# Kernel optimization log

Measured on AMD Instinct MI355X. Metric: run time of the kernel, lower is better.

The kernel has to match this reference:

```python
import jax, jax.numpy as jnp
import numpy as np

CH, HEADS, DH, NMEM, GROUPS, EPS = 128, 4, 32, 4, 32, 1e-5
HID = HEADS * DH

def group_norm(x, w, b):
    # x: [B,C,D,H,W], normalize per group of channels over (C//G, D, H, W)
    B, C = x.shape[0], x.shape[1]
    xg = x.reshape(B, GROUPS, -1)
    mu = xg.mean(axis=-1, keepdims=True)
    var = xg.var(axis=-1, keepdims=True)
    xg = (xg - mu) * jax.lax.rsqrt(var + EPS)
    x = xg.reshape(x.shape)
    return x * w[None, :, None, None, None] + b[None, :, None, None, None]

def setup_inputs() -> dict:
    key = jax.random.key(0)
    ks = jax.random.split(key, 8)
    B, D, H, W = 2, 16, 64, 64
    x = jax.random.normal(ks[0], (B, CH, D, H, W), dtype=jnp.float32)
    norm1_w = jnp.ones((CH,), jnp.float32)
    norm1_b = jnp.zeros((CH,), jnp.float32)
    w_qkv = jax.random.normal(ks[1], (3 * HID, CH), dtype=jnp.float32) * (CH ** -0.5)
    mem_kv = jax.random.normal(ks[2], (2, HEADS, DH, NMEM), dtype=jnp.float32)
    w_out = jax.random.normal(ks[3], (CH, HID), dtype=jnp.float32) * (HID ** -0.5)
    b_out = jnp.zeros((CH,), jnp.float32)
    norm2_w = jnp.ones((CH,), jnp.float32)
    norm2_b = jnp.zeros((CH,), jnp.float32)
    return {"x": x, "norm1_w": norm1_w, "norm1_b": norm1_b, "w_qkv": w_qkv,
            "mem_kv": mem_kv, "w_out": w_out, "b_out": b_out,
            "norm2_w": norm2_w, "norm2_b": norm2_b}

def reference(x, norm1_w, norm1_b, w_qkv, mem_kv, w_out, b_out, norm2_w, norm2_b):
    B, C, D, H, W = x.shape
    n = D * H * W
    scale = DH ** -0.5
    xn = group_norm(x, norm1_w, norm1_b)
    # 1x1x1 conv == channel matmul: [B,3*HID,n]
    qkv = jnp.einsum('oc,bcn->bon', w_qkv, xn.reshape(B, C, n))
    qkv = qkv.reshape(B, 3, HEADS, DH, n)
    q, k, v = qkv[:, 0], qkv[:, 1], qkv[:, 2]  # [B,HEADS,DH,n]
    mk = jnp.broadcast_to(mem_kv[0][None], (B, HEADS, DH, NMEM))
    mv = jnp.broadcast_to(mem_kv[1][None], (B, HEADS, DH, NMEM))
    k = jnp.concatenate([mk, k], axis=-1)
    v = jnp.concatenate([mv, v], axis=-1)
    q = jax.nn.softmax(q, axis=-2) * scale   # over dim_head
    k = jax.nn.softmax(k, axis=-1)           # over sequence
    context = jnp.einsum('bhdn,bhen->bhde', k, v)  # [B,HEADS,DH,DH]
    out = jnp.einsum('bhde,bhdn->bhen', context, q)  # [B,HEADS,DH,n]
    out = out.reshape(B, HID, D, H, W)
    out = jnp.einsum('oc,bcdhw->bodhw', w_out, out) + b_out[None, :, None, None, None]
    return group_norm(out, norm2_w, norm2_b)
```

## Files before the change

kernel.cpp:

```cpp
#include <hip/hip_runtime.h>
#include <math.h>

#define CH     128
#define EPSV   1e-5f
#define SCALE  0.17677669529663687f
#define GSIZE  262144.0f

typedef short bf16x8 __attribute__((ext_vector_type(8)));
typedef short bf16x4 __attribute__((ext_vector_type(4)));
typedef float f32x4  __attribute__((ext_vector_type(4)));

__device__ __forceinline__ unsigned cvtpk(float lo, float hi) {
    unsigned r;
    asm("v_cvt_pk_bf16_f32 %0, %1, %2" : "=v"(r) : "v"(lo), "v"(hi));
    return r;
}
__device__ __forceinline__ unsigned short f2bf(float f) {
    unsigned u = __float_as_uint(f);
    u += 0x7FFF + ((u >> 16) & 1);
    return (unsigned short)(u >> 16);
}
__device__ __forceinline__ float bf2f(unsigned short s) {
    return __uint_as_float(((unsigned)s) << 16);
}

__global__ __launch_bounds__(256) void gn_partial(const float* __restrict__ x,
                                                  float* __restrict__ part) {
    __shared__ float s1[256], s2[256];
    int t = threadIdx.x;
    const float4* xp = (const float4*)(x + (size_t)blockIdx.x * 8192);
    float s = 0.f, q = 0.f;
#pragma unroll
    for (int i = 0; i < 8; ++i) {
        float4 v = xp[t + 256 * i];
        s += v.x + v.y + v.z + v.w;
        q += v.x * v.x + v.y * v.y + v.z * v.z + v.w * v.w;
    }
    s1[t] = s; s2[t] = q;
    __syncthreads();
    for (int st = 128; st > 0; st >>= 1) {
        if (t < st) { s1[t] += s1[t + st]; s2[t] += s2[t + st]; }
        __syncthreads();
    }
    if (t == 0) { part[2 * blockIdx.x] = s1[0]; part[2 * blockIdx.x + 1] = s2[0]; }
}

__global__ void prep1(const float* __restrict__ part, float* __restrict__ mu, float* __restrict__ rs) {
    int t = threadIdx.x;
    float s = 0.f, q = 0.f;
    for (int i = 0; i < 32; ++i) { s += part[2*(t*32+i)]; q += part[2*(t*32+i)+1]; }
    float m = s * (1.f / GSIZE);
    float v = q * (1.f / GSIZE) - m * m;
    mu[t] = m; rs[t] = rsqrtf(v + EPSV);
}

__global__ __launch_bounds__(256) void kv_pass(const float* __restrict__ x,
        const float* __restrict__ w_qkv,
        const float* __restrict__ n1w, const float* __restrict__ n1b,
        const float* __restrict__ mu, const float* __restrict__ rs,
        float* __restrict__ part_kv) {
    __shared__ short xk[16*64*8];
    __shared__ short kvstage[8*256*8];
    int tid = threadIdx.x;
    int l = tid & 63, w = tid >> 6;
    int ncol = l & 15, kg = l >> 4;
    int b = blockIdx.x >> 8;
    int h = w;

    bf16x8 afrag[4][4];
    {
        int row0 = 128 + w*64 + ncol;
        int k0   = 8 * kg;
#pragma unroll
        for (int rt = 0; rt < 4; ++rt)
#pragma unroll
        for (int ks = 0; ks < 4; ++ks) {
            const float* p = w_qkv + (size_t)(row0 + 16*rt)*CH + k0 + 32*ks;
            float4 u0 = *(const float4*)p;
            float4 u1 = *(const float4*)(p + 4);
            bf16x8 f;
            f[0]=(short)f2bf(u0.x); f[1]=(short)f2bf(u0.y); f[2]=(short)f2bf(u0.z); f[3]=(short)f2bf(u0.w);
            f[4]=(short)f2bf(u1.x); f[5]=(short)f2bf(u1.y); f[6]=(short)f2bf(u1.z); f[7]=(short)f2bf(u1.w);
            afrag[rt][ks] = f;
        }
    }

    int nst = (tid & 15) * 4;
    int cst = (tid >> 4) * 8;
    float aa[8], bb[8];
#pragma unroll
    for (int i = 0; i < 8; ++i) {
        int c = cst + i;
        int fg = b*32 + (c >> 2);
        float a0 = rs[fg] * n1w[c];
        aa[i] = a0;
        bb[i] = n1b[c] - mu[fg] * a0;
    }

    f32x4 cc[2][2];
#pragma unroll
    for (int i = 0; i < 2; ++i)
#pragma unroll
    for (int j = 0; j < 2; ++j)
#pragma unroll
    for (int q = 0; q < 4; ++q) cc[i][j][q] = 0.f;
    float zacc[2] = {0.f, 0.f};

    float4 xv[8];
    {
        int n0 = ((blockIdx.x * 4) << 6) & 65535;
#pragma unroll
        for (int i = 0; i < 8; ++i)
            xv[i] = *(const float4*)(x + ((size_t)(b*CH + cst + i) << 16) + n0 + nst);
        const float* xf = (const float*)xv;
#pragma unroll
        for (int j = 0; j < 4; ++j) {
            bf16x8 f;
#pragma unroll
            for (int i = 0; i < 8; ++i)
                f[i] = (short)f2bf(xf[i*4 + j] * aa[i] + bb[i]);
            *(bf16x8*)&xk[((cst >> 3)*64 + nst + j) * 8] = f;
        }
    }

    for (int t4 = 0; t4 < 4; ++t4) {
        __syncthreads();

        f32x4 acc[4][4];
#pragma unroll
        for (int i = 0; i < 4; ++i)
#pragma unroll
        for (int j = 0; j < 4; ++j)
#pragma unroll
        for (int q = 0; q < 4; ++q) acc[i][j][q] = 0.f;

#pragma unroll
        for (int ks = 0; ks < 4; ++ks) {
            bf16x8 bfr[4];
#pragma unroll
            for (int ct = 0; ct < 4; ++ct)
                bfr[ct] = *(bf16x8*)&xk[((4*ks + kg)*64 + 16*ct + ncol) * 8];
#pragma unroll
            for (int rt = 0; rt < 4; ++rt)
#pragma unroll
            for (int ct = 0; ct < 4; ++ct)
                acc[rt][ct] = __builtin_amdgcn_mfma_f32_16x16x32_bf16(
                    afrag[rt][ks], bfr[ct], acc[rt][ct], 0, 0, 0);
        }

#pragma unroll
        for (int rt = 0; rt < 4; ++rt)
#pragma unroll
        for (int ct = 0; ct < 4; ++ct) {
            float v0 = acc[rt][ct][0], v1 = acc[rt][ct][1];
            float v2 = acc[rt][ct][2], v3 = acc[rt][ct][3];
            if (w < 2) { v0 = __expf(v0); v1 = __expf(v1); v2 = __expf(v2); v3 = __expf(v3); }
            unsigned p01 = cvtpk(v0, v1), p23 = cvtpk(v2, v3);
            unsigned short sv[4] = {(unsigned short)p01, (unsigned short)(p01 >> 16),
                                    (unsigned short)p23, (unsigned short)(p23 >> 16)};
            int n = 16*ct + ncol;
#pragma unroll
            for (int q = 0; q < 4; ++q) {
                int row = w*64 + 16*rt + 4*kg + q;
                int byteoff = ((n >> 3)*4096 + row*16 + (n & 7)*2) ^ (((row >> 2) & 3) << 4);
                *(unsigned short*)((char*)kvstage + byteoff) = sv[q];
            }
        }
        __syncthreads();

        if (t4 < 3) {
            int n0 = ((blockIdx.x * 4 + t4 + 1) << 6) & 65535;
#pragma unroll
            for (int i = 0; i < 8; ++i)
                xv[i] = *(const float4*)(x + ((size_t)(b*CH + cst + i) << 16) + n0 + nst);
        }

#pragma unroll
        for (int ks = 0; ks < 2; ++ks) {
            bf16x8 ak[2], bv[2];
#pragma unroll
            for (int rt = 0; rt < 2; ++rt) {
                int row = h*32 + 16*rt + ncol;
                int byteoff = ((4*ks + kg)*4096 + row*16) ^ (((row >> 2) & 3) << 4);
                ak[rt] = *(bf16x8*)((char*)kvstage + byteoff);
            }
#pragma unroll
            for (int ct = 0; ct < 2; ++ct) {
                int row = 128 + h*32 + 16*ct + ncol;
                int byteoff = ((4*ks + kg)*4096 + row*16) ^ (((row >> 2) & 3) << 4);
                bv[ct] = *(bf16x8*)((char*)kvstage + byteoff);
            }
#pragma unroll
            for (int rt = 0; rt < 2; ++rt)
#pragma unroll
            for (int j = 0; j < 8; ++j) zacc[rt] += bf2f((unsigned short)ak[rt][j]);
#pragma unroll
            for (int rt = 0; rt < 2; ++rt)
#pragma unroll
            for (int ct = 0; ct < 2; ++ct)
                cc[rt][ct] = __builtin_amdgcn_mfma_f32_16x16x32_bf16(
                    ak[rt], bv[ct], cc[rt][ct], 0, 0, 0);
        }

        if (t4 < 3) {
            const float* xf = (const float*)xv;
#pragma unroll
            for (int j = 0; j < 4; ++j) {
                bf16x8 f;
#pragma unroll
                for (int i = 0; i < 8; ++i)
                    f[i] = (short)f2bf(xf[i*4 + j] * aa[i] + bb[i]);
                *(bf16x8*)&xk[((cst >> 3)*64 + nst + j) * 8] = f;
            }
        }
    }

    float* dst = part_kv + (size_t)blockIdx.x * 4224;
#pragma unroll
    for (int rt = 0; rt < 2; ++rt)
#pragma unroll
    for (int ct = 0; ct < 2; ++ct)
#pragma unroll
    for (int q = 0; q < 4; ++q) {
        int d = 16*rt + 4*kg + q;
        int e = 16*ct + ncol;
        dst[h*1024 + d*32 + e] = cc[rt][ct][q];
    }
#pragma unroll
    for (int rt = 0; rt < 2; ++rt) {
        zacc[rt] += __shfl_xor(zacc[rt], 16);
        zacc[rt] += __shfl_xor(zacc[rt], 32);
    }
    if (kg == 0) {
        dst[4096 + h*32 + ncol]      = zacc[0];
        dst[4096 + h*32 + 16 + ncol] = zacc[1];
    }
}

__global__ __launch_bounds__(256) void reduce_ctx(const float* __restrict__ part_kv,
                                                  const float* __restrict__ mem_kv,
                                                  float* __restrict__ ctx, float* __restrict__ Z) {
    int gid = blockIdx.x * 256 + threadIdx.x;
    int oi = gid >> 2, sub = gid & 3;
    int b = oi / 4224;
    int e = oi - b * 4224;
    const float* p = part_kv + (size_t)b * 256 * 4224 + e;
    float s = 0.f;
    for (int i = sub; i < 256; i += 4) s += p[(size_t)i * 4224];
    s += __shfl_xor(s, 1);
    s += __shfl_xor(s, 2);
    if (sub == 0) {
        if (e < 4096) {
            int hh = e >> 10, d = (e >> 5) & 31, ee = e & 31;
            float init = 0.f;
            for (int m = 0; m < 4; ++m)
                init += expf(mem_kv[hh*128 + d*4 + m]) * mem_kv[512 + hh*128 + ee*4 + m];
            ctx[b*4096 + e] = init + s;
        } else {
            int d2 = e - 4096;
            float init = 0.f;
            for (int m = 0; m < 4; ++m) init += expf(mem_kv[d2*4 + m]);
            Z[b*128 + d2] = init + s;
        }
    }
}

template<bool BF16OUT>
__global__ __launch_bounds__(256) void out_pass(const float* __restrict__ x,
        const float* __restrict__ w_qkv,
        const float* __restrict__ n1w, const float* __restrict__ n1b,
        const float* __restrict__ mu, const float* __restrict__ rs,
        const float* __restrict__ ctx, const float* __restrict__ Z,
        const float* __restrict__ w_out, const float* __restrict__ b_out,
        float* __restrict__ out, unsigned short* __restrict__ outb,
        float* __restrict__ part2) {
    __shared__ short xk[16*64*8];
    __shared__ short pb[16*64*8];
    int tid = threadIdx.x;
    int l = tid & 63, w = tid >> 6;
    int ncol = l & 15, kg = l >> 4;
    int b = blockIdx.x >> 8;

    bf16x8 aq[2][4], aw[2][4];
#pragma unroll
    for (int rt = 0; rt < 2; ++rt)
#pragma unroll
    for (int ks = 0; ks < 4; ++ks) {
        const float* pq = w_qkv + (size_t)(32*w + 16*rt + ncol)*CH + 8*kg + 32*ks;
        const float* pw = w_out + (size_t)(32*w + 16*rt + ncol)*CH + 8*kg + 32*ks;
        float4 u0 = *(const float4*)pq, u1 = *(const float4*)(pq + 4);
        float4 v0 = *(const float4*)pw, v1 = *(const float4*)(pw + 4);
        bf16x8 fq, fw;
        fq[0]=(short)f2bf(u0.x); fq[1]=(short)f2bf(u0.y); fq[2]=(short)f2bf(u0.z); fq[3]=(short)f2bf(u0.w);
        fq[4]=(short)f2bf(u1.x); fq[5]=(short)f2bf(u1.y); fq[6]=(short)f2bf(u1.z); fq[7]=(short)f2bf(u1.w);
        fw[0]=(short)f2bf(v0.x); fw[1]=(short)f2bf(v0.y); fw[2]=(short)f2bf(v0.z); fw[3]=(short)f2bf(v0.w);
        fw[4]=(short)f2bf(v1.x); fw[5]=(short)f2bf(v1.y); fw[6]=(short)f2bf(v1.z); fw[7]=(short)f2bf(v1.w);
        aq[rt][ks] = fq;
        aw[rt][ks] = fw;
    }

    bf16x8 actx[2];
#pragma unroll
    for (int rt = 0; rt < 2; ++rt) {
        bf16x8 f;
#pragma unroll
        for (int j = 0; j < 8; ++j) {
            int d = 8*kg + j;
            float cv = ctx[b*4096 + w*1024 + d*32 + 16*rt + ncol] / Z[b*128 + w*32 + d];
            f[j] = (short)f2bf(cv);
        }
        actx[rt] = f;
    }

    float bo[2][4];
#pragma unroll
    for (int rt = 0; rt < 2; ++rt)
#pragma unroll
    for (int q = 0; q < 4; ++q)
        bo[rt][q] = b_out[32*w + 16*rt + 4*kg + q];

    int nst = (tid & 15) * 4;
    int cst = (tid >> 4) * 8;
    float aa[8], bb[8];
#pragma unroll
    for (int i = 0; i < 8; ++i) {
        int c = cst + i;
        int fg = b*32 + (c >> 2);
        float a0 = rs[fg] * n1w[c];
        aa[i] = a0;
        bb[i] = n1b[c] - mu[fg] * a0;
    }

    float pgs[2] = {0.f, 0.f}, pgq[2] = {0.f, 0.f};
    float4 xv[8];

    {
        int n0 = (blockIdx.x << 8) & 65535;
#pragma unroll
        for (int i = 0; i < 8; ++i)
            xv[i] = *(const float4*)(x + ((size_t)(b*CH + cst + i) << 16) + n0 + nst);
        const float* xf = (const float*)xv;
#pragma unroll
        for (int j = 0; j < 4; ++j) {
            bf16x8 f;
#pragma unroll
            for (int i = 0; i < 8; ++i)
                f[i] = (short)f2bf(xf[i*4 + j] * aa[i] + bb[i]);
            *(bf16x8*)&xk[((cst >> 3)*64 + nst + j) * 8] = f;
        }
    }

    for (int t4 = 0; t4 < 4; ++t4) {
        int n0 = ((blockIdx.x*4 + t4) << 6) & 65535;
        __syncthreads();

        f32x4 acc[2][4];
#pragma unroll
        for (int i = 0; i < 2; ++i)
#pragma unroll
        for (int j = 0; j < 4; ++j)
#pragma unroll
        for (int q = 0; q < 4; ++q) acc[i][j][q] = 0.f;
#pragma unroll
        for (int ks = 0; ks < 4; ++ks) {
            bf16x8 bfr[4];
#pragma unroll
            for (int ct = 0; ct < 4; ++ct)
                bfr[ct] = *(bf16x8*)&xk[((4*ks + kg)*64 + 16*ct + ncol) * 8];
#pragma unroll
            for (int rt = 0; rt < 2; ++rt)
#pragma unroll
            for (int ct = 0; ct < 4; ++ct)
                acc[rt][ct] = __builtin_amdgcn_mfma_f32_16x16x32_bf16(
                    aq[rt][ks], bfr[ct], acc[rt][ct], 0, 0, 0);
        }

        {
            float sum[4];
#pragma unroll
            for (int ct = 0; ct < 4; ++ct) {
                float s = 0.f;
#pragma unroll
                for (int rt = 0; rt < 2; ++rt)
#pragma unroll
                for (int q = 0; q < 4; ++q) {
                    float e = __expf(acc[rt][ct][q]);
                    acc[rt][ct][q] = e;
                    s += e;
                }
                s += __shfl_xor(s, 16);
                s += __shfl_xor(s, 32);
                sum[ct] = SCALE / s;
            }
#pragma unroll
            for (int ct = 0; ct < 4; ++ct)
#pragma unroll
            for (int rt = 0; rt < 2; ++rt) {
                bf16x4 pk;
#pragma unroll
                for (int q = 0; q < 4; ++q) pk[q] = (short)f2bf(acc[rt][ct][q] * sum[ct]);
                int row0 = w*32 + 16*rt + 4*kg;
                *(bf16x4*)&pb[((row0 >> 3)*64 + 16*ct + ncol)*8 + (row0 & 7)] = pk;
            }
        }

        f32x4 hacc[2][4];
#pragma unroll
        for (int i = 0; i < 2; ++i)
#pragma unroll
        for (int j = 0; j < 4; ++j)
#pragma unroll
        for (int q = 0; q < 4; ++q) hacc[i][j][q] = 0.f;
        {
            bf16x8 bq[4];
#pragma unroll
            for (int ct = 0; ct < 4; ++ct)
                bq[ct] = *(bf16x8*)&pb[((w*4 + kg)*64 + 16*ct + ncol) * 8];
#pragma unroll
            for (int rt = 0; rt < 2; ++rt)
#pragma unroll
            for (int ct = 0; ct < 4; ++ct)
                hacc[rt][ct] = __builtin_amdgcn_mfma_f32_16x16x32_bf16(
                    actx[rt], bq[ct], hacc[rt][ct], 0, 0, 0);
        }

#pragma unroll
        for (int ct = 0; ct < 4; ++ct)
#pragma unroll
        for (int rt = 0; rt < 2; ++rt) {
            bf16x4 pk;
#pragma unroll
            for (int q = 0; q < 4; ++q) pk[q] = (short)f2bf(hacc[rt][ct][q]);
            int row0 = w*32 + 16*rt + 4*kg;
            *(bf16x4*)&pb[((row0 >> 3)*64 + 16*ct + ncol)*8 + (row0 & 7)] = pk;
        }
        __syncthreads();

        if (t4 < 3) {
            int n1 = ((blockIdx.x*4 + t4 + 1) << 6) & 65535;
#pragma unroll
            for (int i = 0; i < 8; ++i)
                xv[i] = *(const float4*)(x + ((size_t)(b*CH + cst + i) << 16) + n1 + nst);
        }

        f32x4 oacc[2][4];
#pragma unroll
        for (int i = 0; i < 2; ++i)
#pragma unroll
        for (int j = 0; j < 4; ++j)
#pragma unroll
        for (int q = 0; q < 4; ++q) oacc[i][j][q] = 0.f;
#pragma unroll
        for (int ks = 0; ks < 4; ++ks) {
            bf16x8 bfr[4];
#pragma unroll
            for (int ct = 0; ct < 4; ++ct)
                bfr[ct] = *(bf16x8*)&pb[((4*ks + kg)*64 + 16*ct + ncol) * 8];
#pragma unroll
            for (int rt = 0; rt < 2; ++rt)
#pragma unroll
            for (int ct = 0; ct < 4; ++ct)
                oacc[rt][ct] = __builtin_amdgcn_mfma_f32_16x16x32_bf16(
                    aw[rt][ks], bfr[ct], oacc[rt][ct], 0, 0, 0);
        }

#pragma unroll
        for (int rt = 0; rt < 2; ++rt)
#pragma unroll
        for (int ct = 0; ct < 4; ++ct)
#pragma unroll
        for (int q = 0; q < 4; ++q) {
            int c = 32*w + 16*rt + 4*kg + q;
            float o = oacc[rt][ct][q] + bo[rt][q];
            size_t idx = ((size_t)(b*CH + c) << 16) + n0 + 16*ct + ncol;
            if (BF16OUT) outb[idx] = f2bf(o);
            else         out[idx] = o;
            pgs[rt] += o;
            pgq[rt] += o*o;
        }

        if (t4 < 3) {
            const float* xf = (const float*)xv;
#pragma unroll
            for (int j = 0; j < 4; ++j) {
                bf16x8 f;
#pragma unroll
                for (int i = 0; i < 8; ++i)
                    f[i] = (short)f2bf(xf[i*4 + j] * aa[i] + bb[i]);
                *(bf16x8*)&xk[((cst >> 3)*64 + nst + j) * 8] = f;
            }
        }
    }

#pragma unroll
    for (int rt = 0; rt < 2; ++rt) {
        float gs = pgs[rt], gq = pgq[rt];
#pragma unroll
        for (int m = 1; m < 16; m <<= 1) {
            gs += __shfl_xor(gs, m);
            gq += __shfl_xor(gq, m);
        }
        if (ncol == 0) {
            int g = 8*w + 4*rt + kg;
            part2[blockIdx.x*64 + g*2 + 0] = gs;
            part2[blockIdx.x*64 + g*2 + 1] = gq;
        }
    }
}

__global__ __launch_bounds__(256) void reduce2(const float* __restrict__ part2,
                                               float* __restrict__ mu, float* __restrict__ rs) {
    __shared__ float s1[256], s2[256];
    int fg = blockIdx.x;
    int b = fg >> 5, g = fg & 31;
    int t = threadIdx.x;
    const float* p = part2 + ((size_t)(b*256 + t))*64 + g*2;
    s1[t] = p[0]; s2[t] = p[1];
    __syncthreads();
    for (int st = 128; st > 0; st >>= 1) {
        if (t < st) { s1[t] += s1[t + st]; s2[t] += s2[t + st]; }
        __syncthreads();
    }
    if (t == 0) {
        float m = s1[0] * (1.f / GSIZE);
        float v = s2[0] * (1.f / GSIZE) - m*m;
        mu[fg] = m; rs[fg] = rsqrtf(v + EPSV);
    }
}

__global__ __launch_bounds__(256) void gn_apply(float* __restrict__ y,
        const float* __restrict__ mu, const float* __restrict__ rs,
        const float* __restrict__ w2, const float* __restrict__ b2) {
    int bi = blockIdx.x, t = threadIdx.x;
    int c = (bi >> 3) & 127;
    int b = bi >> 10;
    int fg = b*32 + (c >> 2);
    float aa = rs[fg] * w2[c];
    float bb = b2[c] - mu[fg] * aa;
    float4* yp = (float4*)(y + (size_t)bi * 8192);
#pragma unroll
    for (int i = 0; i < 8; ++i) {
        float4 v = yp[t + 256*i];
        v.x = v.x*aa+bb; v.y = v.y*aa+bb; v.z = v.z*aa+bb; v.w = v.w*aa+bb;
        yp[t + 256*i] = v;
    }
}

__global__ __launch_bounds__(256) void gn_apply_bf16(const unsigned short* __restrict__ src,
        float* __restrict__ y,
        const float* __restrict__ mu, const float* __restrict__ rs,
        const float* __restrict__ w2, const float* __restrict__ b2) {
    int bi = blockIdx.x, t = threadIdx.x;
    int c = (bi >> 3) & 127;
    int b = bi >> 10;
    int fg = b*32 + (c >> 2);
    float aa = rs[fg] * w2[c];
    float bb = b2[c] - mu[fg] * aa;
    const ushort4* sp = (const ushort4*)(src + (size_t)bi * 8192);
    float4* yp = (float4*)(y + (size_t)bi * 8192);
#pragma unroll
    for (int i = 0; i < 8; ++i) {
        ushort4 u = sp[t + 256*i];
        float4 v;
        v.x = bf2f(u.x)*aa+bb; v.y = bf2f(u.y)*aa+bb;
        v.z = bf2f(u.z)*aa+bb; v.w = bf2f(u.w)*aa+bb;
        yp[t + 256*i] = v;
    }
}

extern "C" void kernel_launch(void* const* d_in, const int* in_sizes, int n_in,
                              void* d_out, int out_size, void* d_ws, size_t ws_size,
                              hipStream_t stream) {
    (void)in_sizes; (void)n_in; (void)out_size;
    const float* x      = (const float*)d_in[0];
    const float* n1w    = (const float*)d_in[1];
    const float* n1b    = (const float*)d_in[2];
    const float* w_qkv  = (const float*)d_in[3];
    const float* mem_kv = (const float*)d_in[4];
    const float* w_out  = (const float*)d_in[5];
    const float* b_out  = (const float*)d_in[6];
    const float* n2w    = (const float*)d_in[7];
    const float* n2b    = (const float*)d_in[8];
    float* out = (float*)d_out;
    float* ws  = (float*)d_ws;

    float* part1   = ws;
    float* mu1     = ws + 4096;
    float* rs1     = ws + 4160;
    float* ctx     = ws + 4224;
    float* Z       = ws + 12416;
    float* part2   = ws + 12672;
    float* mu2     = ws + 143744;
    float* rs2     = ws + 143808;
    float* part_kv = ws + 143872;
    const size_t base_floats = 143872 + (size_t)512*4224;
    unsigned short* outb = (unsigned short*)(ws + base_floats);
    const size_t need = base_floats*4 + (size_t)2*CH*65536*2;
    bool bf16path = ws_size >= need;

    gn_partial<<<2048, 256, 0, stream>>>(x, part1);
    prep1<<<1, 64, 0, stream>>>(part1, mu1, rs1);
    kv_pass<<<512, 256, 0, stream>>>(x, w_qkv, n1w, n1b, mu1, rs1, part_kv);
    reduce_ctx<<<132, 256, 0, stream>>>(part_kv, mem_kv, ctx, Z);
    if (bf16path) {
        out_pass<true><<<512, 256, 0, stream>>>(x, w_qkv, n1w, n1b, mu1, rs1, ctx, Z,
                                                w_out, b_out, out, outb, part2);
        reduce2<<<64, 256, 0, stream>>>(part2, mu2, rs2);
        gn_apply_bf16<<<2048, 256, 0, stream>>>(outb, out, mu2, rs2, n2w, n2b);
    } else {
        out_pass<false><<<512, 256, 0, stream>>>(x, w_qkv, n1w, n1b, mu1, rs1, ctx, Z,
                                                 w_out, b_out, out, outb, part2);
        reduce2<<<64, 256, 0, stream>>>(part2, mu2, rs2);
        gn_apply<<<2048, 256, 0, stream>>>(out, mu2, rs2, n2w, n2b);
    }
}
```

Measured before the change: 135.3 us.

## Fold GroupNorm affine into QKV weights and per-row bias; use packed bf16 converts

The per-channel GroupNorm scale is folded into the bf16 QKV weight fragments, and the shift becomes a per-output-row bias computed once per block and kept in shared memory. The raw x tile then only needs a packed bf16 conversion per element instead of an FMA plus manual rounding, and the bias is added to the MFMA accumulators before exp/softmax. Manual f2bf rounding is replaced by the hardware v_cvt_pk_bf16_f32 packed convert in several places. The trade-off is extra setup work per block, a small shared array, and slightly different rounding, since unnormalized x and scaled weights are quantized to bf16 separately, which could lose accuracy when group statistics are large.

```diff
diff --git a/kernel.cpp b/kernel.cpp
--- a/kernel.cpp
+++ b/kernel.cpp
@@ -14,6 +14,16 @@
     unsigned r;
     asm("v_cvt_pk_bf16_f32 %0, %1, %2" : "=v"(r) : "v"(lo), "v"(hi));
     return r;
+}
+__device__ __forceinline__ bf16x4 pk4(unsigned p01, unsigned p23) {
+    union { unsigned u[2]; bf16x4 v; } t;
+    t.u[0] = p01; t.u[1] = p23;
+    return t.v;
+}
+__device__ __forceinline__ bf16x8 pk8(unsigned a, unsigned b, unsigned c, unsigned d) {
+    union { unsigned u[4]; bf16x8 v; } t;
+    t.u[0] = a; t.u[1] = b; t.u[2] = c; t.u[3] = d;
+    return t.v;
 }
 __device__ __forceinline__ unsigned short f2bf(float f) {
     unsigned u = __float_as_uint(f);
@@ -61,6 +71,7 @@
         float* __restrict__ part_kv) {
     __shared__ short xk[16*64*8];
     __shared__ short kvstage[8*256*8];
+    __shared__ float betas[256];
     int tid = threadIdx.x;
     int l = tid & 63, w = tid >> 6;
     int ncol = l & 15, kg = l >> 4;
@@ -68,34 +79,41 @@
     int h = w;
 
     bf16x8 afrag[4][4];
-    {
-        int row0 = 128 + w*64 + ncol;
-        int k0   = 8 * kg;
-#pragma unroll
-        for (int rt = 0; rt < 4; ++rt)
-#pragma unroll
-        for (int ks = 0; ks < 4; ++ks) {
-            const float* p = w_qkv + (size_t)(row0 + 16*rt)*CH + k0 + 32*ks;
-            float4 u0 = *(const float4*)p;
-            float4 u1 = *(const float4*)(p + 4);
-            bf16x8 f;
-            f[0]=(short)f2bf(u0.x); f[1]=(short)f2bf(u0.y); f[2]=(short)f2bf(u0.z); f[3]=(short)f2bf(u0.w);
-            f[4]=(short)f2bf(u1.x); f[5]=(short)f2bf(u1.y); f[6]=(short)f2bf(u1.z); f[7]=(short)f2bf(u1.w);
-            afrag[rt][ks] = f;
-        }
+    float bsum[4] = {0.f, 0.f, 0.f, 0.f};
+#pragma unroll
+    for (int ks = 0; ks < 4; ++ks) {
+        float a0[8], b0[8];
+#pragma unroll
+        for (int j = 0; j < 8; ++j) {
+            int c = 8*kg + 32*ks + j;
+            int fg = b*32 + (c >> 2);
+            float av = rs[fg] * n1w[c];
+            a0[j] = av;
+            b0[j] = n1b[c] - mu[fg] * av;
+        }
+#pragma unroll
+        for (int rt = 0; rt < 4; ++rt) {
+            const float* p = w_qkv + (size_t)(128 + w*64 + 16*rt + ncol)*CH + 8*kg + 32*ks;
+            float4 u0 = *(const float4*)p, u1 = *(const float4*)(p + 4);
+            float wv[8] = {u0.x,u0.y,u0.z,u0.w,u1.x,u1.y,u1.z,u1.w};
+            afrag[rt][ks] = pk8(cvtpk(wv[0]*a0[0], wv[1]*a0[1]), cvtpk(wv[2]*a0[2], wv[3]*a0[3]),
+                                cvtpk(wv[4]*a0[4], wv[5]*a0[5]), cvtpk(wv[6]*a0[6], wv[7]*a0[7]));
+#pragma unroll
+            for (int j = 0; j < 8; ++j) bsum[rt] += wv[j] * b0[j];
+        }
+    }
+#pragma unroll
+    for (int rt = 0; rt < 4; ++rt) {
+        bsum[rt] += __shfl_xor(bsum[rt], 16);
+        bsum[rt] += __shfl_xor(bsum[rt], 32);
+    }
+    if (kg == 0) {
+#pragma unroll
+        for (int rt = 0; rt < 4; ++rt) betas[w*64 + 16*rt + ncol] = bsum[rt];
     }
 
     int nst = (tid & 15) * 4;
     int cst = (tid >> 4) * 8;
-    float aa[8], bb[8];
-#pragma unroll
-    for (int i = 0; i < 8; ++i) {
-        int c = cst + i;
-        int fg = b*32 + (c >> 2);
-        float a0 = rs[fg] * n1w[c];
-        aa[i] = a0;
-        bb[i] = n1b[c] - mu[fg] * a0;
-    }
 
     f32x4 cc[2][2];
 #pragma unroll
@@ -114,13 +132,10 @@
             xv[i] = *(const float4*)(x + ((size_t)(b*CH + cst + i) << 16) + n0 + nst);
         const float* xf = (const float*)xv;
 #pragma unroll
-        for (int j = 0; j < 4; ++j) {
-            bf16x8 f;
-#pragma unroll
-            for (int i = 0; i < 8; ++i)
-                f[i] = (short)f2bf(xf[i*4 + j] * aa[i] + bb[i]);
-            *(bf16x8*)&xk[((cst >> 3)*64 + nst + j) * 8] = f;
-        }
+        for (int j = 0; j < 4; ++j)
+            *(bf16x8*)&xk[((cst >> 3)*64 + nst + j) * 8] =
+                pk8(cvtpk(xf[0*4+j], xf[1*4+j]), cvtpk(xf[2*4+j], xf[3*4+j]),
+                    cvtpk(xf[4*4+j], xf[5*4+j]), cvtpk(xf[6*4+j], xf[7*4+j]));
     }
 
     for (int t4 = 0; t4 < 4; ++t4) {
@@ -149,21 +164,25 @@
         }
 
 #pragma unroll
-        for (int rt = 0; rt < 4; ++rt)
-#pragma unroll
-        for (int ct = 0; ct < 4; ++ct) {
-            float v0 = acc[rt][ct][0], v1 = acc[rt][ct][1];
-            float v2 = acc[rt][ct][2], v3 = acc[rt][ct][3];
-            if (w < 2) { v0 = __expf(v0); v1 = __expf(v1); v2 = __expf(v2); v3 = __expf(v3); }
-            unsigned p01 = cvtpk(v0, v1), p23 = cvtpk(v2, v3);
-            unsigned short sv[4] = {(unsigned short)p01, (unsigned short)(p01 >> 16),
-                                    (unsigned short)p23, (unsigned short)(p23 >> 16)};
-            int n = 16*ct + ncol;
-#pragma unroll
-            for (int q = 0; q < 4; ++q) {
-                int row = w*64 + 16*rt + 4*kg + q;
-                int byteoff = ((n >> 3)*4096 + row*16 + (n & 7)*2) ^ (((row >> 2) & 3) << 4);
-                *(unsigned short*)((char*)kvstage + byteoff) = sv[q];
+        for (int rt = 0; rt < 4; ++rt) {
+            int lrow0 = w*64 + 16*rt + 4*kg;
+            float be0 = betas[lrow0+0], be1 = betas[lrow0+1];
+            float be2 = betas[lrow0+2], be3 = betas[lrow0+3];
+#pragma unroll
+            for (int ct = 0; ct < 4; ++ct) {
+                float v0 = acc[rt][ct][0] + be0, v1 = acc[rt][ct][1] + be1;
+                float v2 = acc[rt][ct][2] + be2, v3 = acc[rt][ct][3] + be3;
+                if (w < 2) { v0 = __expf(v0); v1 = __expf(v1); v2 = __expf(v2); v3 = __expf(v3); }
+                unsigned p01 = cvtpk(v0, v1), p23 = cvtpk(v2, v3);
+                unsigned short sv[4] = {(unsigned short)p01, (unsigned short)(p01 >> 16),
+                                        (unsigned short)p23, (unsigned short)(p23 >> 16)};
+                int n = 16*ct + ncol;
+#pragma unroll
+                for (int q = 0; q < 4; ++q) {
+                    int row = lrow0 + q;
+                    int byteoff = ((n >> 3)*4096 + row*16 + (n & 7)*2) ^ (((row >> 2) & 3) << 4);
+                    *(unsigned short*)((char*)kvstage + byteoff) = sv[q];
+                }
             }
         }
         __syncthreads();
@@ -205,13 +224,10 @@
         if (t4 < 3) {
             const float* xf = (const float*)xv;
 #pragma unroll
-            for (int j = 0; j < 4; ++j) {
-                bf16x8 f;
-#pragma unroll
-                for (int i = 0; i < 8; ++i)
-                    f[i] = (short)f2bf(xf[i*4 + j] * aa[i] + bb[i]);
-                *(bf16x8*)&xk[((cst >> 3)*64 + nst + j) * 8] = f;
-            }
+            for (int j = 0; j < 4; ++j)
+                *(bf16x8*)&xk[((cst >> 3)*64 + nst + j) * 8] =
+                    pk8(cvtpk(xf[0*4+j], xf[1*4+j]), cvtpk(xf[2*4+j], xf[3*4+j]),
+                        cvtpk(xf[4*4+j], xf[5*4+j]), cvtpk(xf[6*4+j], xf[7*4+j]));
         }
     }
 
@@ -276,27 +292,49 @@
         float* __restrict__ part2) {
     __shared__ short xk[16*64*8];
     __shared__ short pb[16*64*8];
+    __shared__ float betasq[128];
     int tid = threadIdx.x;
     int l = tid & 63, w = tid >> 6;
     int ncol = l & 15, kg = l >> 4;
     int b = blockIdx.x >> 8;
 
     bf16x8 aq[2][4], aw[2][4];
-#pragma unroll
-    for (int rt = 0; rt < 2; ++rt)
+    float bsq[2] = {0.f, 0.f};
 #pragma unroll
     for (int ks = 0; ks < 4; ++ks) {
-        const float* pq = w_qkv + (size_t)(32*w + 16*rt + ncol)*CH + 8*kg + 32*ks;
-        const float* pw = w_out + (size_t)(32*w + 16*rt + ncol)*CH + 8*kg + 32*ks;
-        float4 u0 = *(const float4*)pq, u1 = *(const float4*)(pq + 4);
-        float4 v0 = *(const float4*)pw, v1 = *(const float4*)(pw + 4);
-        bf16x8 fq, fw;
-        fq[0]=(short)f2bf(u0.x); fq[1]=(short)f2bf(u0.y); fq[2]=(short)f2bf(u0.z); fq[3]=(short)f2bf(u0.w);
-        fq[4]=(short)f2bf(u1.x); fq[5]=(short)f2bf(u1.y); fq[6]=(short)f2bf(u1.z); fq[7]=(short)f2bf(u1.w);
-        fw[0]=(short)f2bf(v0.x); fw[1]=(short)f2bf(v0.y); fw[2]=(short)f2bf(v0.z); fw[3]=(short)f2bf(v0.w);
-        fw[4]=(short)f2bf(v1.x); fw[5]=(short)f2bf(v1.y); fw[6]=(short)f2bf(v1.z); fw[7]=(short)f2bf(v1.w);
-        aq[rt][ks] = fq;
-        aw[rt][ks] = fw;
+        float a0[8], b0[8];
+#pragma unroll
+        for (int j = 0; j < 8; ++j) {
+            int c = 8*kg + 32*ks + j;
+            int fg = b*32 + (c >> 2);
+            float av = rs[fg] * n1w[c];
+            a0[j] = av;
+            b0[j] = n1b[c] - mu[fg] * av;
+        }
+#pragma unroll
+        for (int rt = 0; rt < 2; ++rt) {
+            const float* pq = w_qkv + (size_t)(32*w + 16*rt + ncol)*CH + 8*kg + 32*ks;
+            const float* pw = w_out + (size_t)(32*w + 16*rt + ncol)*CH + 8*kg + 32*ks;
+            float4 u0 = *(const float4*)pq, u1 = *(const float4*)(pq + 4);
+            float4 v0 = *(const float4*)pw, v1 = *(const float4*)(pw + 4);
+            float wq[8] = {u0.x,u0.y,u0.z,u0.w,u1.x,u1.y,u1.z,u1.w};
+            float wo[8] = {v0.x,v0.y,v0.z,v0.w,v1.x,v1.y,v1.z,v1.w};
+            aq[rt][ks] = pk8(cvtpk(wq[0]*a0[0], wq[1]*a0[1]), cvtpk(wq[2]*a0[2], wq[3]*a0[3]),
+                             cvtpk(wq[4]*a0[4], wq[5]*a0[5]), cvtpk(wq[6]*a0[6], wq[7]*a0[7]));
+            aw[rt][ks] = pk8(cvtpk(wo[0], wo[1]), cvtpk(wo[2], wo[3]),
+                             cvtpk(wo[4], wo[5]), cvtpk(wo[6], wo[7]));
+#pragma unroll
+            for (int j = 0; j < 8; ++j) bsq[rt] += wq[j] * b0[j];
+        }
+    }
+#pragma unroll
+    for (int rt = 0; rt < 2; ++rt) {
+        bsq[rt] += __shfl_xor(bsq[rt], 16);
+        bsq[rt] += __shfl_xor(bsq[rt], 32);
+    }
+    if (kg == 0) {
+#pragma unroll
+        for (int rt = 0; rt < 2; ++rt) betasq[32*w + 16*rt + ncol] = bsq[rt];
     }
 
     bf16x8 actx[2];
@@ -321,16 +359,6 @@
 
     int nst = (tid & 15) * 4;
     int cst = (tid >> 4) * 8;
-    float aa[8], bb[8];
-#pragma unroll
-    for (int i = 0; i < 8; ++i) {
-        int c = cst + i;
-        int fg = b*32 + (c >> 2);
-        float a0 = rs[fg] * n1w[c];
-        aa[i] = a0;
-        bb[i] = n1b[c] - mu[fg] * a0;
-    }
-
     float pgs[2] = {0.f, 0.f}, pgq[2] = {0.f, 0.f};
     float4 xv[8];
 
@@ -341,13 +369,10 @@
             xv[i] = *(const float4*)(x + ((size_t)(b*CH + cst + i) << 16) + n0 + nst);
         const float* xf = (const float*)xv;
 #pragma unroll
-        for (int j = 0; j < 4; ++j) {
-            bf16x8 f;
-#pragma unroll
-            for (int i = 0; i < 8; ++i)
-                f[i] = (short)f2bf(xf[i*4 + j] * aa[i] + bb[i]);
-            *(bf16x8*)&xk[((cst >> 3)*64 + nst + j) * 8] = f;
-        }
+        for (int j = 0; j < 4; ++j)
+            *(bf16x8*)&xk[((cst >> 3)*64 + nst + j) * 8] =
+                pk8(cvtpk(xf[0*4+j], xf[1*4+j]), cvtpk(xf[2*4+j], xf[3*4+j]),
+                    cvtpk(xf[4*4+j], xf[5*4+j]), cvtpk(xf[6*4+j], xf[7*4+j]));
     }
 
     for (int t4 = 0; t4 < 4; ++t4) {
@@ -376,6 +401,11 @@
         }
 
         {
+            float be[2][4];
+#pragma unroll
+            for (int rt = 0; rt < 2; ++rt)
+#pragma unroll
+            for (int q = 0; q < 4; ++q) be[rt][q] = betasq[32*w + 16*rt + 4*kg + q];
             float sum[4];
 #pragma unroll
             for (int ct = 0; ct < 4; ++ct) {
@@ -384,7 +414,7 @@
                 for (int rt = 0; rt < 2; ++rt)
 #pragma unroll
                 for (int q = 0; q < 4; ++q) {
-                    float e = __expf(acc[rt][ct][q]);
+                    float e = __expf(acc[rt][ct][q] + be[rt][q]);
                     acc[rt][ct][q] = e;
                     s += e;
                 }
@@ -396,11 +426,10 @@
             for (int ct = 0; ct < 4; ++ct)
 #pragma unroll
             for (int rt = 0; rt < 2; ++rt) {
-                bf16x4 pk;
-#pragma unroll
-                for (int q = 0; q < 4; ++q) pk[q] = (short)f2bf(acc[rt][ct][q] * sum[ct]);
+                unsigned p01 = cvtpk(acc[rt][ct][0]*sum[ct], acc[rt][ct][1]*sum[ct]);
+                unsigned p23 = cvtpk(acc[rt][ct][2]*sum[ct], acc[rt][ct][3]*sum[ct]);
                 int row0 = w*32 + 16*rt + 4*kg;
-                *(bf16x4*)&pb[((row0 >> 3)*64 + 16*ct + ncol)*8 + (row0 & 7)] = pk;
+                *(bf16x4*)&pb[((row0 >> 3)*64 + 16*ct + ncol)*8 + (row0 & 7)] = pk4(p01, p23);
             }
         }
 
@@ -428,11 +457,10 @@
         for (int ct = 0; ct < 4; ++ct)
 #pragma unroll
         for (int rt = 0; rt < 2; ++rt) {
-            bf16x4 pk;
-#pragma unroll
-            for (int q = 0; q < 4; ++q) pk[q] = (short)f2bf(hacc[rt][ct][q]);
+            unsigned p01 = cvtpk(hacc[rt][ct][0], hacc[rt][ct][1]);
+            unsigned p23 = cvtpk(hacc[rt][ct][2], hacc[rt][ct][3]);
             int row0 = w*32 + 16*rt + 4*kg;
-            *(bf16x4*)&pb[((row0 >> 3)*64 + 16*ct + ncol)*8 + (row0 & 7)] = pk;
+            *(bf16x4*)&pb[((row0 >> 3)*64 + 16*ct + ncol)*8 + (row0 & 7)] = pk4(p01, p23);
         }
         __syncthreads();
 
@@ -482,13 +510,10 @@
         if (t4 < 3) {
             const float* xf = (const float*)xv;
 #pragma unroll
-            for (int j = 0; j < 4; ++j) {
-                bf16x8 f;
-#pragma unroll
-                for (int i = 0; i < 8; ++i)
-                    f[i] = (short)f2bf(xf[i*4 + j] * aa[i] + bb[i]);
-                *(bf16x8*)&xk[((cst >> 3)*64 + nst + j) * 8] = f;
-            }
+            for (int j = 0; j < 4; ++j)
+                *(bf16x8*)&xk[((cst >> 3)*64 + nst + j) * 8] =
+                    pk8(cvtpk(xf[0*4+j], xf[1*4+j]), cvtpk(xf[2*4+j], xf[3*4+j]),
+                        cvtpk(xf[4*4+j], xf[5*4+j]), cvtpk(xf[6*4+j], xf[7*4+j]));
         }
     }
 
```

After: 131.5 us. 1.03x faster.
